# Performance work log

Hardware: AMD Instinct MI355X
Metric: run time of the kernel (lower is better)

The kernel has to match this reference:

```python
import jax, jax.numpy as jnp
import numpy as np

# NAM: in_features independent 1->H->H->1 MLPs (FeatureNNs), batched over the
# feature dimension F instead of a Python loop of tiny kernels.
# inputs: (B, F); W1,b1: (F, H); W2: (F, H, H); b2: (F, H); W3: (F, H); b3: (F,)

def setup_inputs() -> dict:
    key = jax.random.key(0)
    ks = jax.random.split(key, 7)
    B, F, H = 8192, 128, 64
    s1 = 1.0  # fan_in = 1 for first layer
    s2 = 1.0 / np.sqrt(H)
    return {
        "inputs": jax.random.normal(ks[0], (B, F), dtype=jnp.float32),
        "W1": jax.random.normal(ks[1], (F, H), dtype=jnp.float32) * s1,
        "b1": jax.random.normal(ks[2], (F, H), dtype=jnp.float32) * 0.01,
        "W2": jax.random.normal(ks[3], (F, H, H), dtype=jnp.float32) * s2,
        "b2": jax.random.normal(ks[4], (F, H), dtype=jnp.float32) * 0.01,
        "W3": jax.random.normal(ks[5], (F, H), dtype=jnp.float32) * s2,
        "b3": jax.random.normal(ks[6], (F,), dtype=jnp.float32) * 0.01,
    }


def reference(inputs, W1, b1, W2, b2, W3, b3):
    # Layer 1: scalar input per feature -> hidden.  (B,F,1)*(F,H) -> (B,F,H)
    h1 = jax.nn.relu(inputs[:, :, None] * W1[None, :, :] + b1[None, :, :])
    # Layer 2: per-feature hidden->hidden batched matmul.
    h2 = jax.nn.relu(jnp.einsum("bfh,fhk->bfk", h1, W2) + b2[None, :, :])
    # Output layer: hidden -> scalar per feature.
    fnn = jnp.einsum("bfh,fh->bf", h2, W3) + b3[None, :]  # (B, F)
    out = fnn.sum(axis=-1)  # (B,)  additive model output
    return (out, fnn)
```

## Files before the change

kernel.cpp:

```cpp
#include <hip/hip_runtime.h>

#define B 8192
#define F 128
#define H 64

typedef __attribute__((ext_vector_type(8))) short bf16x8;
typedef __attribute__((ext_vector_type(4))) float f32x4;

static __device__ __forceinline__ unsigned short f32_to_bf16_rne(float v) {
    unsigned int u = __float_as_uint(v);
    unsigned int r = (u + 0x7FFFu + ((u >> 16) & 1u)) >> 16;
    return (unsigned short)r;
}
static __device__ __forceinline__ float bf16_to_f32(unsigned short h) {
    return __uint_as_float(((unsigned int)h) << 16);
}

#define GLOAD_LDS16(gp, lp)                                                  \
    __builtin_amdgcn_global_load_lds(                                        \
        (const __attribute__((address_space(1))) unsigned int*)(gp),         \
        (__attribute__((address_space(3))) unsigned int*)(lp), 16, 0, 0)


__global__ __launch_bounds__(256) void nam_prep(
    const float* __restrict__ W2, short* __restrict__ bhi_g,
    short* __restrict__ blo_g)
{
    const int tid = threadIdx.x;
    const int f = blockIdx.x;
    const float* W2f = W2 + (size_t)f * H * H;
    short* bhi = bhi_g + (size_t)f * 4096;
    short* blo = blo_g + (size_t)f * 4096;
#pragma unroll
    for (int t = tid; t < 512; t += 256) {
        const int n = t & 63;
        const int g = t >> 6;
        const int nt = n >> 4, c = n & 15;
        const int ks = g >> 2, q = g & 3;
        const int slot = (nt * 2 + ks) * 64 + c + 16 * q;
        bf16x8 hv, lv;
#pragma unroll
        for (int jj = 0; jj < 8; ++jj) {
            const float wv = W2f[(g * 8 + jj) * H + n];
            const unsigned short hi = f32_to_bf16_rne(wv);
            const unsigned short lo = f32_to_bf16_rne(wv - bf16_to_f32(hi));
            hv[jj] = (short)hi;
            lv[jj] = (short)lo;
        }
        *(bf16x8*)&bhi[slot * 8] = hv;
        *(bf16x8*)&blo[slot * 8] = lv;
    }
}

__global__ __launch_bounds__(256, 3) void nam_main(
    const float* __restrict__ inputs, const float* __restrict__ W1,
    const float* __restrict__ b1, const short* __restrict__ bhi_g,
    const short* __restrict__ blo_g, const float* __restrict__ b2,
    const float* __restrict__ W3, const float* __restrict__ b3,
    float* __restrict__ fnn_ws)
{
    const int tid = threadIdx.x;
    const int f = blockIdx.y;
    const int b0 = blockIdx.x * 512;

    const int lane = tid & 63;
    const int w    = tid >> 6;
    const int q    = lane >> 4;
    const int col  = lane & 15;

    __shared__ __align__(16) short bhs[4096];
    __shared__ __align__(16) short bls[4096];
    {
        const short* bhi_f = bhi_g + (size_t)f * 4096;
        const short* blo_f = blo_g + (size_t)f * 4096;
#pragma unroll
        for (int c = w; c < 8; c += 4) {
            GLOAD_LDS16(bhi_f + c * 512 + lane * 8, &bhs[c * 512]);
            GLOAD_LDS16(blo_f + c * 512 + lane * 8, &bls[c * 512]);
        }
    }

    const float* W1f = W1 + f * H;
    const float* b1f = b1 + f * H;
    float w1v[16], b1v[16];
#pragma unroll
    for (int ks = 0; ks < 2; ++ks)
#pragma unroll
        for (int j = 0; j < 8; ++j) {
            w1v[ks * 8 + j] = W1f[ks * 32 + q * 8 + j];
            b1v[ks * 8 + j] = b1f[ks * 32 + q * 8 + j];
        }
    const float* b2f = b2 + f * H;
    const float* W3f = W3 + f * H;
    float b2v[4], w3v[4];
#pragma unroll
    for (int nt = 0; nt < 4; ++nt) {
        b2v[nt] = b2f[nt * 16 + col];
        w3v[nt] = W3f[nt * 16 + col];
    }
    const float b3f = b3[f];

    const int rowbase = b0 + w * 128 + col;
    float x_next = inputs[(size_t)rowbase * F + f];

    __syncthreads();

    bf16x8 bhi[4][2], blo[4][2];
#pragma unroll
    for (int nt = 0; nt < 4; ++nt)
#pragma unroll
        for (int ks = 0; ks < 2; ++ks) {
            const int slot = (nt * 2 + ks) * 64 + lane;
            bhi[nt][ks] = *(bf16x8*)&bhs[slot * 8];
            blo[nt][ks] = *(bf16x8*)&bls[slot * 8];
        }

#pragma unroll 1
    for (int mt = 0; mt < 8; ++mt) {
        const int rbase = b0 + w * 128 + mt * 16;
        const float x = x_next;
        if (mt < 7)
            x_next = inputs[(size_t)(rowbase + (mt + 1) * 16) * F + f];

        f32x4 acc[4];
#pragma unroll
        for (int nt = 0; nt < 4; ++nt) {
            acc[nt][0] = b2v[nt]; acc[nt][1] = b2v[nt];
            acc[nt][2] = b2v[nt]; acc[nt][3] = b2v[nt];
        }

#pragma unroll
        for (int ks = 0; ks < 2; ++ks) {
            union { unsigned int u[4]; bf16x8 v; } Ah, Al;
#pragma unroll
            for (int t = 0; t < 4; ++t) {
                const float r0 = fmaxf(fmaf(x, w1v[ks * 8 + 2 * t],     b1v[ks * 8 + 2 * t]),     0.0f);
                const float r1 = fmaxf(fmaf(x, w1v[ks * 8 + 2 * t + 1], b1v[ks * 8 + 2 * t + 1]), 0.0f);
                const unsigned int u0 = __float_as_uint(r0);
                const unsigned int u1 = __float_as_uint(r1);
                const float l0 = r0 - __uint_as_float(u0 & 0xFFFF0000u);
                const float l1 = r1 - __uint_as_float(u1 & 0xFFFF0000u);
                Ah.u[t] = __builtin_amdgcn_perm(u1, u0, 0x07060302);
                Al.u[t] = __builtin_amdgcn_perm(__float_as_uint(l1),
                                                __float_as_uint(l0), 0x07060302);
            }
#pragma unroll
            for (int nt = 0; nt < 4; ++nt) {
                acc[nt] = __builtin_amdgcn_mfma_f32_16x16x32_bf16(Ah.v, bhi[nt][ks], acc[nt], 0, 0, 0);
                acc[nt] = __builtin_amdgcn_mfma_f32_16x16x32_bf16(Ah.v, blo[nt][ks], acc[nt], 0, 0, 0);
                acc[nt] = __builtin_amdgcn_mfma_f32_16x16x32_bf16(Al.v, bhi[nt][ks], acc[nt], 0, 0, 0);
            }
        }

        float s[4];
#pragma unroll
        for (int reg = 0; reg < 4; ++reg) {
            float t = 0.0f;
#pragma unroll
            for (int nt = 0; nt < 4; ++nt)
                t = fmaf(fmaxf(acc[nt][reg], 0.0f), w3v[nt], t);
            s[reg] = t;
        }
#pragma unroll
        for (int m_ = 1; m_ <= 8; m_ <<= 1)
#pragma unroll
            for (int reg = 0; reg < 4; ++reg)
                s[reg] += __shfl_xor(s[reg], m_, 64);
        if (col == 0) {
            f32x4 o;
            o[0] = s[0] + b3f; o[1] = s[1] + b3f;
            o[2] = s[2] + b3f; o[3] = s[3] + b3f;
            *(f32x4*)&fnn_ws[(size_t)f * B + rbase + 4 * q] = o;
        }
    }
}

__global__ __launch_bounds__(256) void nam_finish(
    const float* __restrict__ fnn_ws, float* __restrict__ fnn,
    float* __restrict__ out)
{
    const int tid = threadIdx.x;
    const int blk = blockIdx.x;
    const int r0 = (blk & 127) * 64;
    const int f0 = (blk >> 7) * 32;
    __shared__ float tile[32][65];
    __shared__ float psum[4][64];

    float rsum = 0.0f;
#pragma unroll
    for (int j = 0; j < 8; ++j) {
        const int fl = j * 4 + (tid >> 6);
        const int rl = tid & 63;
        const float v = fnn_ws[(size_t)(f0 + fl) * B + r0 + rl];
        tile[fl][rl] = v;
        rsum += v;
    }
    psum[tid >> 6][tid & 63] = rsum;
    __syncthreads();
    if (tid < 64) {
        const float s = psum[0][tid] + psum[1][tid] + psum[2][tid] + psum[3][tid];
        atomicAdd(&out[r0 + tid], s);
    }
#pragma unroll
    for (int j = 0; j < 8; ++j) {
        const int rl = j * 8 + (tid >> 5);
        const int fl = tid & 31;
        fnn[(size_t)(r0 + rl) * F + f0 + fl] = tile[fl][rl];
    }
}

__global__ __launch_bounds__(256, 3) void nam_mono(
    const float* __restrict__ inputs, const float* __restrict__ W1,
    const float* __restrict__ b1, const float* __restrict__ W2,
    const float* __restrict__ b2, const float* __restrict__ W3,
    const float* __restrict__ b3, float* __restrict__ out,
    float* __restrict__ fnn_out)
{
    const int tid = threadIdx.x;
    const int f = blockIdx.y;
    const int b0 = blockIdx.x * 256;

    const float* W1f = W1 + f * H;
    const float* b1f = b1 + f * H;
    const float* W2f = W2 + (size_t)f * H * H;
    const float* b2f = b2 + f * H;
    const float* W3f = W3 + f * H;

    __shared__ __align__(16) short bhi_s[512 * 8];
    __shared__ __align__(16) short blo_s[512 * 8];

#pragma unroll
    for (int t = tid; t < 512; t += 256) {
        const int n = t & 63;
        const int g = t >> 6;
        const int nt = n >> 4, c = n & 15;
        const int ks = g >> 2, q = g & 3;
        const int slot = (nt * 2 + ks) * 64 + c + 16 * q;
        bf16x8 hv, lv;
#pragma unroll
        for (int jj = 0; jj < 8; ++jj) {
            const float wv = W2f[(g * 8 + jj) * H + n];
            const unsigned short hi = f32_to_bf16_rne(wv);
            const unsigned short lo = f32_to_bf16_rne(wv - bf16_to_f32(hi));
            hv[jj] = (short)hi;
            lv[jj] = (short)lo;
        }
        *(bf16x8*)&bhi_s[slot * 8] = hv;
        *(bf16x8*)&blo_s[slot * 8] = lv;
    }

    const int lane = tid & 63;
    const int w    = tid >> 6;
    const int q    = lane >> 4;
    const int col  = lane & 15;

    float w1v[16], b1v[16];
#pragma unroll
    for (int ks = 0; ks < 2; ++ks)
#pragma unroll
        for (int j = 0; j < 8; ++j) {
            w1v[ks * 8 + j] = W1f[ks * 32 + q * 8 + j];
            b1v[ks * 8 + j] = b1f[ks * 32 + q * 8 + j];
        }
    float b2v[4], w3v[4];
#pragma unroll
    for (int nt = 0; nt < 4; ++nt) {
        b2v[nt] = b2f[nt * 16 + col];
        w3v[nt] = W3f[nt * 16 + col];
    }
    const float b3f = b3[f];

    float x4[4];
#pragma unroll
    for (int mt = 0; mt < 4; ++mt)
        x4[mt] = inputs[(size_t)(b0 + w * 64 + mt * 16 + col) * F + f];

    __syncthreads();

    bf16x8 bhi[4][2], blo[4][2];
#pragma unroll
    for (int nt = 0; nt < 4; ++nt)
#pragma unroll
        for (int ks = 0; ks < 2; ++ks) {
            const int slot = (nt * 2 + ks) * 64 + lane;
            bhi[nt][ks] = *(bf16x8*)&bhi_s[slot * 8];
            blo[nt][ks] = *(bf16x8*)&blo_s[slot * 8];
        }

#pragma unroll 1
    for (int mt = 0; mt < 4; ++mt) {
        const int rbase = b0 + w * 64 + mt * 16;
        const float x = x4[mt];

        f32x4 acc[4];
#pragma unroll
        for (int nt = 0; nt < 4; ++nt) {
            acc[nt][0] = b2v[nt]; acc[nt][1] = b2v[nt];
            acc[nt][2] = b2v[nt]; acc[nt][3] = b2v[nt];
        }

#pragma unroll
        for (int ks = 0; ks < 2; ++ks) {
            union { unsigned int u[4]; bf16x8 v; } Ah, Al;
#pragma unroll
            for (int t = 0; t < 4; ++t) {
                const float r0 = fmaxf(fmaf(x, w1v[ks * 8 + 2 * t],     b1v[ks * 8 + 2 * t]),     0.0f);
                const float r1 = fmaxf(fmaf(x, w1v[ks * 8 + 2 * t + 1], b1v[ks * 8 + 2 * t + 1]), 0.0f);
                const unsigned int u0 = __float_as_uint(r0);
                const unsigned int u1 = __float_as_uint(r1);
                const float l0 = r0 - __uint_as_float(u0 & 0xFFFF0000u);
                const float l1 = r1 - __uint_as_float(u1 & 0xFFFF0000u);
                Ah.u[t] = __builtin_amdgcn_perm(u1, u0, 0x07060302);
                Al.u[t] = __builtin_amdgcn_perm(__float_as_uint(l1),
                                                __float_as_uint(l0), 0x07060302);
            }
#pragma unroll
            for (int nt = 0; nt < 4; ++nt) {
                acc[nt] = __builtin_amdgcn_mfma_f32_16x16x32_bf16(Ah.v, bhi[nt][ks], acc[nt], 0, 0, 0);
                acc[nt] = __builtin_amdgcn_mfma_f32_16x16x32_bf16(Ah.v, blo[nt][ks], acc[nt], 0, 0, 0);
                acc[nt] = __builtin_amdgcn_mfma_f32_16x16x32_bf16(Al.v, bhi[nt][ks], acc[nt], 0, 0, 0);
            }
        }

        float s[4];
#pragma unroll
        for (int reg = 0; reg < 4; ++reg) {
            float t = 0.0f;
#pragma unroll
            for (int nt = 0; nt < 4; ++nt)
                t = fmaf(fmaxf(acc[nt][reg], 0.0f), w3v[nt], t);
            s[reg] = t;
        }
#pragma unroll
        for (int m_ = 1; m_ <= 8; m_ <<= 1)
#pragma unroll
            for (int reg = 0; reg < 4; ++reg)
                s[reg] += __shfl_xor(s[reg], m_, 64);
        if (col == 0) {
#pragma unroll
            for (int reg = 0; reg < 4; ++reg) {
                const int row = rbase + 4 * q + reg;
                const float val = s[reg] + b3f;
                fnn_out[(size_t)row * F + f] = val;
                atomicAdd(&out[row], val);
            }
        }
    }
}

extern "C" void kernel_launch(void* const* d_in, const int* in_sizes, int n_in,
                              void* d_out, int out_size, void* d_ws, size_t ws_size,
                              hipStream_t stream) {
    const float* inputs = (const float*)d_in[0];
    const float* W1     = (const float*)d_in[1];
    const float* b1     = (const float*)d_in[2];
    const float* W2     = (const float*)d_in[3];
    const float* b2     = (const float*)d_in[4];
    const float* W3     = (const float*)d_in[5];
    const float* b3     = (const float*)d_in[6];

    float* out = (float*)d_out;
    float* fnn = out + B;

    const size_t WS_NEEDED = (size_t)F * 4096 * 2 * sizeof(short)
                           + (size_t)F * B * sizeof(float);

    hipMemsetAsync(out, 0, B * sizeof(float), stream);

    if (ws_size >= WS_NEEDED) {
        short* bhi_g = (short*)d_ws;
        short* blo_g = bhi_g + (size_t)F * 4096;
        float* fnw   = (float*)(blo_g + (size_t)F * 4096);

        nam_prep<<<dim3(F), 256, 0, stream>>>(W2, bhi_g, blo_g);
        nam_main<<<dim3(B / 512, F), 256, 0, stream>>>(inputs, W1, b1, bhi_g,
                                                       blo_g, b2, W3, b3, fnw);
        nam_finish<<<dim3(512), 256, 0, stream>>>(fnw, fnn, out);
    } else {
        nam_mono<<<dim3(B / 256, F), 256, 0, stream>>>(inputs, W1, b1, W2, b2,
                                                       W3, b3, out, fnn);
    }
}
```

Measured before the change: 107.9 us.

## Replace shuffle reduction with LDS tile reduction and drop atomics in finish kernel

In nam_main, each wave's per-column partial sums now go into an LDS tile instead of a 4-stage cross-lane shuffle reduction. After the loop, each lane sums one row over 16 columns and writes the results out coalesced. nam_finish now has each block cover all 128 features for 64 rows, so the row sum is written directly and needs neither atomicAdd nor the leading hipMemsetAsync. It also writes fnn with 16-byte vector stores. The trade-offs are a larger LDS footprint in nam_main, which may reduce occupancy, and fewer, heavier finish blocks with possible LDS bank conflicts on the strided tile reads.

```diff
diff --git a/kernel.cpp b/kernel.cpp
--- a/kernel.cpp
+++ b/kernel.cpp
@@ -68,8 +68,10 @@
     const int q    = lane >> 4;
     const int col  = lane & 15;
 
+    __shared__ float s_tile[4][128][18];
     __shared__ __align__(16) short bhs[4096];
     __shared__ __align__(16) short bls[4096];
+
     {
         const short* bhi_f = bhi_g + (size_t)f * 4096;
         const short* blo_f = blo_g + (size_t)f * 4096;
@@ -117,7 +119,6 @@
 
 #pragma unroll 1
     for (int mt = 0; mt < 8; ++mt) {
-        const int rbase = b0 + w * 128 + mt * 16;
         const float x = x_next;
         if (mt < 7)
             x_next = inputs[(size_t)(rowbase + (mt + 1) * 16) * F + f];
@@ -152,26 +153,26 @@
             }
         }
 
-        float s[4];
 #pragma unroll
         for (int reg = 0; reg < 4; ++reg) {
             float t = 0.0f;
 #pragma unroll
             for (int nt = 0; nt < 4; ++nt)
                 t = fmaf(fmaxf(acc[nt][reg], 0.0f), w3v[nt], t);
-            s[reg] = t;
-        }
-#pragma unroll
-        for (int m_ = 1; m_ <= 8; m_ <<= 1)
-#pragma unroll
-            for (int reg = 0; reg < 4; ++reg)
-                s[reg] += __shfl_xor(s[reg], m_, 64);
-        if (col == 0) {
-            f32x4 o;
-            o[0] = s[0] + b3f; o[1] = s[1] + b3f;
-            o[2] = s[2] + b3f; o[3] = s[3] + b3f;
-            *(f32x4*)&fnn_ws[(size_t)f * B + rbase + 4 * q] = o;
-        }
+            s_tile[w][mt * 16 + 4 * q + reg][col] = t;
+        }
+    }
+
+    {
+        float sum0 = 0.0f, sum1 = 0.0f;
+#pragma unroll
+        for (int c = 0; c < 16; ++c) {
+            sum0 += s_tile[w][lane][c];
+            sum1 += s_tile[w][lane + 64][c];
+        }
+        float* dst = fnn_ws + (size_t)f * B + b0 + w * 128;
+        dst[lane]      = sum0 + b3f;
+        dst[lane + 64] = sum1 + b3f;
     }
 }
 
@@ -180,32 +181,34 @@
     float* __restrict__ out)
 {
     const int tid = threadIdx.x;
-    const int blk = blockIdx.x;
-    const int r0 = (blk & 127) * 64;
-    const int f0 = (blk >> 7) * 32;
-    __shared__ float tile[32][65];
+    const int r0 = blockIdx.x * 64;
+    __shared__ float tile[128][65];
     __shared__ float psum[4][64];
 
     float rsum = 0.0f;
 #pragma unroll
-    for (int j = 0; j < 8; ++j) {
+    for (int j = 0; j < 32; ++j) {
         const int fl = j * 4 + (tid >> 6);
         const int rl = tid & 63;
-        const float v = fnn_ws[(size_t)(f0 + fl) * B + r0 + rl];
+        const float v = fnn_ws[(size_t)fl * B + r0 + rl];
         tile[fl][rl] = v;
         rsum += v;
     }
     psum[tid >> 6][tid & 63] = rsum;
     __syncthreads();
-    if (tid < 64) {
-        const float s = psum[0][tid] + psum[1][tid] + psum[2][tid] + psum[3][tid];
-        atomicAdd(&out[r0 + tid], s);
-    }
+    if (tid < 64)
+        out[r0 + tid] = psum[0][tid] + psum[1][tid] + psum[2][tid] + psum[3][tid];
+
 #pragma unroll
     for (int j = 0; j < 8; ++j) {
         const int rl = j * 8 + (tid >> 5);
-        const int fl = tid & 31;
-        fnn[(size_t)(r0 + rl) * F + f0 + fl] = tile[fl][rl];
+        const int c4 = tid & 31;
+        f32x4 v;
+        v[0] = tile[c4 * 4 + 0][rl];
+        v[1] = tile[c4 * 4 + 1][rl];
+        v[2] = tile[c4 * 4 + 2][rl];
+        v[3] = tile[c4 * 4 + 3][rl];
+        *(f32x4*)&fnn[(size_t)(r0 + rl) * F + c4 * 4] = v;
     }
 }
 
@@ -365,8 +368,6 @@
     const size_t WS_NEEDED = (size_t)F * 4096 * 2 * sizeof(short)
                            + (size_t)F * B * sizeof(float);
 
-    hipMemsetAsync(out, 0, B * sizeof(float), stream);
-
     if (ws_size >= WS_NEEDED) {
         short* bhi_g = (short*)d_ws;
         short* blo_g = bhi_g + (size_t)F * 4096;
@@ -375,8 +376,9 @@
         nam_prep<<<dim3(F), 256, 0, stream>>>(W2, bhi_g, blo_g);
         nam_main<<<dim3(B / 512, F), 256, 0, stream>>>(inputs, W1, b1, bhi_g,
                                                        blo_g, b2, W3, b3, fnw);
-        nam_finish<<<dim3(512), 256, 0, stream>>>(fnw, fnn, out);
+        nam_finish<<<dim3(128), 256, 0, stream>>>(fnw, fnn, out);
     } else {
+        hipMemsetAsync(out, 0, B * sizeof(float), stream);
         nam_mono<<<dim3(B / 256, F), 256, 0, stream>>>(inputs, W1, b1, W2, b2,
                                                        W3, b3, out, fnn);
     }
```

Result: faster. 100.8 us (-6.5%).
